# Kernel tuning notes

Measured on AMD Instinct MI355X. Metric: run time of the kernel, lower is better.

The kernel has to match this reference:

```python
import jax, jax.numpy as jnp
import numpy as np

B, S, DIM = 4, 3968, 512
H, HD = 8, 64
CHUNK, NPM, MEM = 496, 32, 1024  # MEM == NPM + 2*CHUNK (required by module's EMA update broadcast)


def _lin(k, din, dout):
    kw, kb = jax.random.split(k)
    w = jax.random.normal(kw, (din, dout), jnp.float32) / np.sqrt(din)
    b = jax.random.normal(kb, (dout,), jnp.float32) * 0.01
    return w, b


def setup_inputs() -> dict:
    key = jax.random.key(0)
    ks = jax.random.split(key, 12)
    inp = {}
    inp["x"] = jax.random.normal(ks[0], (B, S, DIM), jnp.float32)
    inp["persistent_memory"] = jax.random.normal(ks[1], (NPM, DIM), jnp.float32)
    # outer query projection
    inp["Wq_out"], inp["bq_out"] = _lin(ks[2], DIM, DIM)
    # NeuralMemory projections
    inp["mk_w"], inp["mk_b"] = _lin(ks[3], DIM, DIM)
    inp["mv_w"], inp["mv_b"] = _lin(ks[4], DIM, DIM)
    inp["mq_w"], inp["mq_b"] = _lin(ks[5], DIM, DIM)
    # TitanAttention (standard MHA: q/k/v to H*HD, out proj back to DIM)
    inp["aq_w"], inp["aq_b"] = _lin(ks[6], DIM, H * HD)
    inp["ak_w"], inp["ak_b"] = _lin(ks[7], DIM, H * HD)
    inp["av_w"], inp["av_b"] = _lin(ks[8], DIM, H * HD)
    inp["ao_w"], inp["ao_b"] = _lin(ks[9], H * HD, DIM)
    return inp


def reference(x, persistent_memory, Wq_out, bq_out,
              mk_w, mk_b, mv_w, mv_b, mq_w, mq_b,
              aq_w, aq_b, ak_w, ak_b, av_w, av_b, ao_w, ao_b):
    Bn, Sn, D = x.shape
    nch = Sn // CHUNK
    inv_sqrt_d = 1.0 / np.sqrt(D).astype(np.float32)
    inv_sqrt_hd = 1.0 / np.sqrt(HD).astype(np.float32)

    def retrieve(mem, q):
        # mem: [B, MEM, D], q: [B, L, D]
        qp = q @ mq_w + mq_b
        k = mem @ mk_w + mk_b
        v = mem @ mv_w + mv_b
        sc = jnp.einsum('bqd,bmd->bqm', qp, k) * inv_sqrt_d
        a = jax.nn.softmax(sc, axis=-1)
        return jnp.einsum('bqm,bmd->bqd', a, v)

    def mha(t):
        # t: [B, L, D] -> [B, L, D]; dropout inactive (eval)
        Bm, L, _ = t.shape
        q = (t @ aq_w + aq_b).reshape(Bm, L, H, HD)
        k = (t @ ak_w + ak_b).reshape(Bm, L, H, HD)
        v = (t @ av_w + av_b).reshape(Bm, L, H, HD)
        sc = jnp.einsum('bqhd,bkhd->bhqk', q, k) * inv_sqrt_hd
        a = jax.nn.softmax(sc, axis=-1)
        o = jnp.einsum('bhqk,bkhd->bqhd', a, v).reshape(Bm, L, H * HD)
        return o @ ao_w + ao_b

    pm = jnp.broadcast_to(persistent_memory[None], (Bn, NPM, D))
    chunks = x.reshape(Bn, nch, CHUNK, D).transpose(1, 0, 2, 3)  # [nch, B, C, D]
    mem0 = jnp.zeros((Bn, MEM, D), x.dtype)

    def step(mem, chunk):
        query = chunk @ Wq_out + bq_out
        hist = retrieve(mem, query)                              # [B, C, D]
        combined = jnp.concatenate([pm, hist, chunk], axis=1)    # [B, MEM, D]
        attended = mha(combined)
        mem2 = 0.9 * mem + 0.1 * attended                        # EMA update
        mout = retrieve(mem2, attended)
        out = (attended * mout)[:, -CHUNK:]                      # keep last chunk slice
        return mem2, out

    _, outs = jax.lax.scan(step, mem0, chunks)                   # outs: [nch, B, C, D]
    return outs.transpose(1, 0, 2, 3).reshape(Bn, Sn, D)
```

## Files before the change

kernel.cpp:

```cpp
#include <hip/hip_runtime.h>
#include <hip/hip_fp16.h>


typedef __attribute__((ext_vector_type(8))) short short8;
typedef __attribute__((ext_vector_type(4))) float f32x4;

static __device__ __forceinline__ unsigned short f32_bf16(float f) {
  unsigned int u = __float_as_uint(f);
  u += 0x7FFFu + ((u >> 16) & 1u);
  return (unsigned short)(u >> 16);
}
static __device__ __forceinline__ float bf_f32(unsigned short h) {
  return __uint_as_float(((unsigned)h) << 16);
}
static __device__ __forceinline__ unsigned pk(float lo, float hi) {
  return (unsigned)f32_bf16(lo) | ((unsigned)f32_bf16(hi) << 16);
}

template<int BM, int BN, int ATY, int BTY, int CTY, bool GUARD, bool BIAS>
__global__ __launch_bounds__(256) void gemm2(
    const void* __restrict__ Ap, long long Asb, long long Ash, int Ars,
    const void* __restrict__ Bp, long long Bsb, long long Bsh, int Brs,
    void* __restrict__ Cp, long long Csb, long long Csh, int Crs,
    void* __restrict__ Cp2, int csplit, void* __restrict__ Cp3,
    const float* __restrict__ bias, float scale, int M, int Kdim, int Hh)
{
  constexpr int LDP = 72;
  constexpr int WN = (BN >= 128) ? 2 : (BM >= 128 ? 1 : 2);
  constexpr int WM = 4 / WN;
  constexpr int MI = BM / (WM * 16);
  constexpr int NI = BN / (WN * 16);
  constexpr int AP = BM / 32;
  constexpr int BP = BN / 32;

  __shared__ unsigned short As[2][BM][LDP];
  __shared__ unsigned short Bs[2][BN][LDP];

  const int tid  = threadIdx.x;
  const int lane = tid & 63;
  const int w    = tid >> 6;
  const int wm   = w / WN, wn = w % WN;
  const int z    = blockIdx.z;
  const int zb   = z / Hh, zh = z - zb * Hh;
  const int m0   = blockIdx.x * BM;
  const int n0   = blockIdx.y * BN;
  const int lrow = lane & 15;
  const int lkB  = (lane >> 4) * 8;
  const int srow = tid >> 3;
  const int scol = (tid & 7) * 8;

  const float*          Af  = (const float*)Ap          + zb * Asb + zh * Ash;
  const unsigned short* Ahp = (const unsigned short*)Ap + zb * Asb + zh * Ash;
  const float*          Bf  = (const float*)Bp          + zb * Bsb + zh * Bsh;
  const unsigned short* Bhp = (const unsigned short*)Bp + zb * Bsb + zh * Bsh;

  float4 afl[AP][2]; uint4 ahl[AP];
  float4 bfl[BP][2]; uint4 bhl[BP];

  auto loadT = [&](int k0) {
    #pragma unroll
    for (int p = 0; p < AP; ++p) {
      const int row = srow + p * 32;
      const bool ok = !GUARD || (m0 + row) < M;
      if constexpr (ATY == 0) {
        if (ok) {
          const float* s = Af + (long long)(m0 + row) * Ars + k0 + scol;
          afl[p][0] = *(const float4*)s;
          afl[p][1] = *(const float4*)(s + 4);
        } else {
          afl[p][0] = make_float4(0.f,0.f,0.f,0.f);
          afl[p][1] = make_float4(0.f,0.f,0.f,0.f);
        }
      } else {
        ahl[p] = ok ? *(const uint4*)(Ahp + (long long)(m0 + row) * Ars + k0 + scol)
                    : make_uint4(0u,0u,0u,0u);
      }
    }
    #pragma unroll
    for (int p = 0; p < BP; ++p) {
      const int row = srow + p * 32;
      if constexpr (BTY == 0) {
        const float* s = Bf + (long long)(n0 + row) * Brs + k0 + scol;
        bfl[p][0] = *(const float4*)s;
        bfl[p][1] = *(const float4*)(s + 4);
      } else {
        bhl[p] = *(const uint4*)(Bhp + (long long)(n0 + row) * Brs + k0 + scol);
      }
    }
  };
  auto writeT = [&](int buf) {
    #pragma unroll
    for (int p = 0; p < AP; ++p) {
      const int row = srow + p * 32;
      uint4 u;
      if constexpr (ATY == 0) {
        u.x = pk(afl[p][0].x, afl[p][0].y); u.y = pk(afl[p][0].z, afl[p][0].w);
        u.z = pk(afl[p][1].x, afl[p][1].y); u.w = pk(afl[p][1].z, afl[p][1].w);
      } else u = ahl[p];
      *(uint4*)(&As[buf][row][scol]) = u;
    }
    #pragma unroll
    for (int p = 0; p < BP; ++p) {
      const int row = srow + p * 32;
      uint4 u;
      if constexpr (BTY == 0) {
        u.x = pk(bfl[p][0].x, bfl[p][0].y); u.y = pk(bfl[p][0].z, bfl[p][0].w);
        u.z = pk(bfl[p][1].x, bfl[p][1].y); u.w = pk(bfl[p][1].z, bfl[p][1].w);
      } else u = bhl[p];
      *(uint4*)(&Bs[buf][row][scol]) = u;
    }
  };

  f32x4 acc[MI][NI] = {};

  loadT(0);
  writeT(0);
  __syncthreads();

  const int NT = Kdim >> 6;
  int cur = 0;
  for (int t = 0; t < NT; ++t) {
    const bool more = (t + 1) < NT;
    if (more) loadT((t + 1) << 6);

    short8 a8[MI][2], b8[NI][2];
    #pragma unroll
    for (int mi = 0; mi < MI; ++mi) {
      const unsigned short* r = &As[cur][wm * (MI * 16) + mi * 16 + lrow][lkB];
      a8[mi][0] = *(const short8*)r;
      a8[mi][1] = *(const short8*)(r + 32);
    }
    #pragma unroll
    for (int ni = 0; ni < NI; ++ni) {
      const unsigned short* r = &Bs[cur][wn * (NI * 16) + ni * 16 + lrow][lkB];
      b8[ni][0] = *(const short8*)r;
      b8[ni][1] = *(const short8*)(r + 32);
    }
    #pragma unroll
    for (int kk = 0; kk < 2; ++kk)
      #pragma unroll
      for (int mi = 0; mi < MI; ++mi)
        #pragma unroll
        for (int ni = 0; ni < NI; ++ni)
          acc[mi][ni] = __builtin_amdgcn_mfma_f32_16x16x32_bf16(a8[mi][kk], b8[ni][kk], acc[mi][ni], 0, 0, 0);

    if (more) writeT(cur ^ 1);
    __syncthreads();
    cur ^= 1;
  }

  float*          Cf  = (float*)Cp          + zb * Csb + zh * Csh;
  unsigned short* Chn = (unsigned short*)Cp + zb * Csb + zh * Csh;
  unsigned short* Ch2 = (unsigned short*)Cp2;
  unsigned short* Kb3 = (unsigned short*)Cp3;
  const bool trside = (CTY == 4 || CTY == 5) ? (n0 >= csplit) : false;

  #pragma unroll
  for (int ni = 0; ni < NI; ++ni) {
    const int col = n0 + wn * (NI * 16) + ni * 16 + lrow;
    const float bv = BIAS ? bias[col] : 0.0f;
    #pragma unroll
    for (int mi = 0; mi < MI; ++mi) {
      const int rbase = m0 + wm * (MI * 16) + mi * 16 + ((lane >> 4) << 2);
      if constexpr (CTY == 5) {
        ushort4 vt;
        #pragma unroll
        for (int r = 0; r < 4; ++r) {
          const int row = rbase + r;
          const float proj = acc[mi][ni][r] * scale + bv;
          const long long midx = (long long)row * Crs + col;
          const float v = 0.9f * Cf[midx] + 0.1f * proj;
          Cf[midx] = v;
          if (!trside) Kb3[(long long)row * 512 + col] = f32_bf16(v);
          else ((unsigned short*)&vt)[r] = f32_bf16(v);
        }
        if (trside)
          *(ushort4*)(&Ch2[(long long)(rbase >> 10) * 524288
                           + (long long)(col - csplit) * 1024 + (rbase & 1023)]) = vt;
      } else if constexpr (CTY == 6) {
        const float* ATTp = (const float*)Cp2;
        float* Of = (float*)Cp;
        #pragma unroll
        for (int r = 0; r < 4; ++r) {
          const int row = rbase + r;
          if (row < M) {
            const float v = acc[mi][ni][r] * scale;
            const float a = ATTp[((long long)zb * 496 + row) * 512 + col];
            Of[((long long)zb * 3968 + (long long)csplit * 496 + row) * 512 + col] = v * a;
          }
        }
      } else if constexpr (CTY == 8) {
        float* ATTo = (float*)Cp2;
        #pragma unroll
        for (int r = 0; r < 4; ++r) {
          const int row = rbase + r;
          if (row < M) {
            const float v = acc[mi][ni][r] * scale + bv;
            if (col < csplit)
              Kb3[((long long)zb * 496 + row) * 512 + col] = f32_bf16(v);
            else
              ATTo[((long long)zb * 496 + row) * 512 + (col - csplit)] = v;
          }
        }
      } else if (trside) {
        ushort4 v;
        v.x = f32_bf16(acc[mi][ni][0] * scale + bv);
        v.y = f32_bf16(acc[mi][ni][1] * scale + bv);
        v.z = f32_bf16(acc[mi][ni][2] * scale + bv);
        v.w = f32_bf16(acc[mi][ni][3] * scale + bv);
        *(ushort4*)(&Ch2[(long long)(rbase >> 10) * 524288
                         + (long long)(col - csplit) * 1024 + (rbase & 1023)]) = v;
      } else {
        #pragma unroll
        for (int r = 0; r < 4; ++r) {
          const int row = rbase + r;
          if (!GUARD || row < M) {
            const float v = acc[mi][ni][r] * scale + bv;
            if constexpr (CTY == 0)      Cf [(long long)row * Crs + col] = v;
            else                         Chn[(long long)row * Crs + col] = f32_bf16(v);
          }
        }
      }
    }
  }
}

__global__ __launch_bounds__(256) void flash_mha_ks(
    const unsigned short* __restrict__ QK, const unsigned short* __restrict__ Vt,
    unsigned short* __restrict__ Opart, float* __restrict__ ML)
{
  __shared__ unsigned short Ks[128][72];
  __shared__ unsigned short Vs[64][136];
  __shared__ unsigned short Ps[64][136];

  const int tid = threadIdx.x, lane = tid & 63, w = tid >> 6;
  const int f = blockIdx.x;
  const int xcd = f & 7, j = f >> 3;
  const int bh = xcd + 8 * (j >> 5);
  const int jj = j & 31;
  const int qt = jj >> 1, part = jj & 1;
  const int b = bh >> 3, h = bh & 7;
  const int q0 = qt * 64, koff = part * 4;
  const unsigned short* Qp = QK + (long long)b * 1048576 + h * 64;
  const unsigned short* Kp = Qp + 512;
  const unsigned short* Vp = Vt + (long long)b * 524288 + (long long)(h * 64) * 1024;

  const int lr = lane & 15, g = lane >> 4, lk = g * 8;
  const int wq = w * 16;

  short8 qb[2];
  qb[0] = *(const short8*)(Qp + (long long)(q0 + wq + lr) * 1024 + lk);
  qb[1] = *(const short8*)(Qp + (long long)(q0 + wq + lr) * 1024 + 32 + lk);

  const int krow = tid >> 1, kcol = (tid & 1) * 32;
  const int vrow = tid >> 2, vcol = (tid & 3) * 32;

  uint4 kl[4], vl[4];
  auto loadKV = [&](int kt) {
    #pragma unroll
    for (int jx = 0; jx < 4; ++jx)
      kl[jx] = *(const uint4*)(Kp + (long long)(kt * 128 + krow) * 1024 + kcol + jx * 8);
    #pragma unroll
    for (int jx = 0; jx < 4; ++jx)
      vl[jx] = *(const uint4*)(Vp + (long long)vrow * 1024 + kt * 128 + vcol + jx * 8);
  };
  auto writeKV = [&]() {
    #pragma unroll
    for (int jx = 0; jx < 4; ++jx) *(uint4*)(&Ks[krow][kcol + jx * 8]) = kl[jx];
    #pragma unroll
    for (int jx = 0; jx < 4; ++jx) *(uint4*)(&Vs[vrow][vcol + jx * 8]) = vl[jx];
  };

  loadKV(koff); writeKV();
  __syncthreads();

  f32x4 acc[4] = {};
  float m = -1e30f, l = 0.f;

  for (int it = 0; it < 4; ++it) {
    const bool more = it < 3;
    if (more) loadKV(koff + it + 1);

    f32x4 s[8] = {};
    #pragma unroll
    for (int ks = 0; ks < 2; ++ks)
      #pragma unroll
      for (int ni = 0; ni < 8; ++ni) {
        const short8 ka = *(const short8*)(&Ks[ni * 16 + lr][ks * 32 + lk]);
        s[ni] = __builtin_amdgcn_mfma_f32_16x16x32_bf16(ka, qb[ks], s[ni], 0, 0, 0);
      }

    float rm = -1e30f;
    #pragma unroll
    for (int ni = 0; ni < 8; ++ni)
      #pragma unroll
      for (int r = 0; r < 4; ++r) { s[ni][r] *= 0.125f; rm = fmaxf(rm, s[ni][r]); }
    rm = fmaxf(rm, __shfl_xor(rm, 16));
    rm = fmaxf(rm, __shfl_xor(rm, 32));

    const float mn = fmaxf(m, rm);
    const float al = __expf(m - mn);
    m = mn;
    float ls = 0.f;
    #pragma unroll
    for (int ni = 0; ni < 8; ++ni)
      #pragma unroll
      for (int r = 0; r < 4; ++r) { s[ni][r] = __expf(s[ni][r] - m); ls += s[ni][r]; }
    ls += __shfl_xor(ls, 16);
    ls += __shfl_xor(ls, 32);
    l = l * al + ls;
    #pragma unroll
    for (int nd = 0; nd < 4; ++nd)
      #pragma unroll
      for (int r = 0; r < 4; ++r) acc[nd][r] *= al;

    #pragma unroll
    for (int ni = 0; ni < 8; ++ni)
      #pragma unroll
      for (int r = 0; r < 4; ++r)
        Ps[wq + lr][ni * 16 + (g << 2) + r] = f32_bf16(s[ni][r]);

    #pragma unroll
    for (int ks2 = 0; ks2 < 4; ++ks2) {
      const short8 pb = *(const short8*)(&Ps[wq + lr][ks2 * 32 + lk]);
      #pragma unroll
      for (int nd = 0; nd < 4; ++nd) {
        const short8 va = *(const short8*)(&Vs[nd * 16 + lr][ks2 * 32 + lk]);
        acc[nd] = __builtin_amdgcn_mfma_f32_16x16x32_bf16(va, pb, acc[nd], 0, 0, 0);
      }
    }

    if (more) { __syncthreads(); writeKV(); __syncthreads(); }
  }

  const int pbq = (bh * 16 + qt) * 2 + part;
  unsigned short* Ob = Opart + (long long)pbq * 4096;
  #pragma unroll
  for (int nd = 0; nd < 4; ++nd)
    #pragma unroll
    for (int r = 0; r < 4; ++r)
      Ob[(16 * nd + 4 * g + r) * 64 + wq + lr] = f32_bf16(acc[nd][r]);
  if (g == 0) {
    ML[pbq * 128 + wq + lr] = m;
    ML[pbq * 128 + 64 + wq + lr] = l;
  }
}

__global__ __launch_bounds__(256) void combine_mha(
    const unsigned short* __restrict__ Opart, const float* __restrict__ ML,
    unsigned short* __restrict__ OH)
{
  __shared__ float Oc[64][65];
  __shared__ float w1s[64], w2s[64], wis[64];
  const int t = threadIdx.x;
  const int bq = blockIdx.x;
  const int bh = bq >> 4, qt = bq & 15, b = bh >> 3, h = bh & 7, q0 = qt * 64;
  const unsigned short* O1 = Opart + (long long)(bq * 2 + 0) * 4096;
  const unsigned short* O2 = Opart + (long long)(bq * 2 + 1) * 4096;
  const float* ml1 = ML + (bq * 2 + 0) * 128;
  const float* ml2 = ML + (bq * 2 + 1) * 128;
  if (t < 64) {
    const float m1 = ml1[t], l1 = ml1[64 + t], m2 = ml2[t], l2 = ml2[64 + t];
    const float mm = fmaxf(m1, m2);
    const float e1 = __expf(m1 - mm), e2 = __expf(m2 - mm);
    w1s[t] = e1; w2s[t] = e2; wis[t] = 1.0f / (e1 * l1 + e2 * l2);
  }
  __syncthreads();
  {
    const int d = t >> 2, qs = (t & 3) * 16;
    const uint4 a0 = *(const uint4*)(O1 + d * 64 + qs);
    const uint4 a1 = *(const uint4*)(O1 + d * 64 + qs + 8);
    const uint4 b0 = *(const uint4*)(O2 + d * 64 + qs);
    const uint4 b1 = *(const uint4*)(O2 + d * 64 + qs + 8);
    const unsigned short* pa = (const unsigned short*)&a0;
    unsigned short ua[16], ub[16];
    *(uint4*)&ua[0] = a0; *(uint4*)&ua[8] = a1;
    *(uint4*)&ub[0] = b0; *(uint4*)&ub[8] = b1;
    #pragma unroll
    for (int i = 0; i < 16; ++i) {
      const int q = qs + i;
      Oc[d][q] = (w1s[q] * bf_f32(ua[i]) + w2s[q] * bf_f32(ub[i])) * wis[q];
    }
  }
  __syncthreads();
  {
    const int q = t >> 2, ds = (t & 3) * 16;
    unsigned short tmp[16];
    #pragma unroll
    for (int i = 0; i < 16; ++i) tmp[i] = f32_bf16(Oc[ds + i][q]);
    unsigned short* dst = OH + (long long)b * 524288 + (long long)(q0 + q) * 512 + h * 64 + ds;
    *(uint4*)dst = *(uint4*)&tmp[0];
    *(uint4*)(dst + 8) = *(uint4*)&tmp[8];
  }
}

struct TP7 { const float* s[7]; unsigned short* d[7]; };
__global__ __launch_bounds__(256) void transpose7(TP7 tp)
{
  __shared__ float tile[32][33];
  const float* in = tp.s[blockIdx.z];
  unsigned short* out = tp.d[blockIdx.z];
  const int c0 = blockIdx.x * 32, r0 = blockIdx.y * 32;
  const int xx = threadIdx.x & 31, ys = threadIdx.x >> 5;
  #pragma unroll
  for (int yy = ys; yy < 32; yy += 8)
    tile[yy][xx] = in[(long long)(r0 + yy) * 512 + c0 + xx];
  __syncthreads();
  #pragma unroll
  for (int yy = ys; yy < 32; yy += 8)
    out[(long long)(c0 + yy) * 512 + r0 + xx] = f32_bf16(tile[xx][yy]);
}

__global__ __launch_bounds__(256) void softmax_rows_bf(
    const float* __restrict__ buf, unsigned short* __restrict__ obuf,
    int rowsPerZ, long long zStride)
{
  const int gr   = blockIdx.x * 4 + (threadIdx.x >> 6);
  const int lane = threadIdx.x & 63;
  const int z = gr / rowsPerZ;
  const int i = gr - z * rowsPerZ;
  const float* pf = buf + (long long)z * zStride + (long long)i * 1024 + lane * 16;
  float v[16];
  #pragma unroll
  for (int j = 0; j < 4; ++j) {
    const float4 f = ((const float4*)pf)[j];
    v[4*j+0] = f.x; v[4*j+1] = f.y; v[4*j+2] = f.z; v[4*j+3] = f.w;
  }
  float mx = v[0];
  #pragma unroll
  for (int j = 1; j < 16; ++j) mx = fmaxf(mx, v[j]);
  #pragma unroll
  for (int d = 32; d; d >>= 1) mx = fmaxf(mx, __shfl_xor(mx, d));
  float s = 0.0f;
  #pragma unroll
  for (int j = 0; j < 16; ++j) { v[j] = __expf(v[j] - mx); s += v[j]; }
  #pragma unroll
  for (int d = 32; d; d >>= 1) s += __shfl_xor(s, d);
  const float inv = 1.0f / s;
  unsigned short* ph = obuf + (long long)z * zStride + (long long)i * 1024 + lane * 16;
  unsigned uu[8];
  #pragma unroll
  for (int j = 0; j < 8; ++j) uu[j] = pk(v[2*j] * inv, v[2*j+1] * inv);
  ((uint4*)ph)[0] = make_uint4(uu[0], uu[1], uu[2], uu[3]);
  ((uint4*)ph)[1] = make_uint4(uu[4], uu[5], uu[6], uu[7]);
}

__global__ __launch_bounds__(256) void copy_pm8(const float* __restrict__ pm, unsigned short* __restrict__ comb8)
{
  const int ci = blockIdx.y;
  const int idx = blockIdx.x * 256 + threadIdx.x;
  const int b = idx >> 11, e = idx & 2047;
  const int row = e >> 6, d8 = (e & 63) * 8;
  const float* s = pm + row * 512 + d8;
  const float4 f0 = *(const float4*)s;
  const float4 f1 = *(const float4*)(s + 4);
  uint4 u; u.x = pk(f0.x, f0.y); u.y = pk(f0.z, f0.w); u.z = pk(f1.x, f1.y); u.w = pk(f1.z, f1.w);
  *(uint4*)(comb8 + (long long)ci * 2097152 + (long long)b * 524288 + row * 512 + d8) = u;
}

__global__ __launch_bounds__(256) void copy_chunk8(const float* __restrict__ x, unsigned short* __restrict__ comb8)
{
  const int ci = blockIdx.y;
  const int idx = blockIdx.x * 256 + threadIdx.x;
  const int b = idx / 31744, e = idx % 31744;
  const int row = e >> 6, d8 = (e & 63) * 8;
  const float* s = x + ((long long)b * 3968 + ci * 496 + row) * 512 + d8;
  const float4 f0 = *(const float4*)s;
  const float4 f1 = *(const float4*)(s + 4);
  uint4 u; u.x = pk(f0.x, f0.y); u.y = pk(f0.z, f0.w); u.z = pk(f1.x, f1.y); u.w = pk(f1.z, f1.w);
  *(uint4*)(comb8 + (long long)ci * 2097152 + (long long)b * 524288 + (528 + row) * 512 + d8) = u;
}

__global__ __launch_bounds__(256) void init_kv(const float* __restrict__ mkb, const float* __restrict__ mvb,
                                               float* __restrict__ master, unsigned short* __restrict__ Kb)
{
  const int idx = blockIdx.x * 256 + threadIdx.x;
  const int c4 = (idx & 255) * 4;
  const long long row = idx >> 8;
  const float4 v = *(const float4*)((c4 < 512) ? (mkb + c4) : (mvb + c4 - 512));
  *(float4*)(master + row * 1024 + c4) = v;
  if (c4 < 512) {
    ushort4 h; h.x = f32_bf16(v.x); h.y = f32_bf16(v.y); h.z = f32_bf16(v.z); h.w = f32_bf16(v.w);
    *(ushort4*)(Kb + row * 512 + c4) = h;
  }
}

__global__ __launch_bounds__(256) void init_vt(const float* __restrict__ mvb, unsigned short* __restrict__ VT)
{
  const int idx = blockIdx.x * 256 + threadIdx.x;
  const int k8 = (idx & 127) * 8;
  const int d  = (idx >> 7) & 511;
  const int b  = idx >> 16;
  const unsigned short hv = f32_bf16(mvb[d]);
  const ushort4 h4 = make_ushort4(hv, hv, hv, hv);
  unsigned short* dst = VT + (long long)b * 524288 + (long long)d * 1024 + k8;
  *(ushort4*)dst = h4; *(ushort4*)(dst + 4) = h4;
}

__global__ __launch_bounds__(256) void fuse_bias(const float* __restrict__ bq, const float* __restrict__ mq,
                                                 const float* __restrict__ mqb, float* __restrict__ bqm)
{
  const int c = blockIdx.x * 256 + threadIdx.x;
  float s = mqb[c];
  for (int j = 0; j < 512; ++j) s += bq[j] * mq[j * 512 + c];
  bqm[c] = s;
}

__global__ __launch_bounds__(256) void fuse_bias2(const float* __restrict__ aob,
                                                  const float* __restrict__ mkw, const float* __restrict__ mkb,
                                                  const float* __restrict__ mvw, const float* __restrict__ mvb,
                                                  float* __restrict__ baokv)
{
  const int c = blockIdx.x * 256 + threadIdx.x;
  const float* w  = (c < 512) ? mkw : mvw;
  const float* bb = (c < 512) ? mkb : mvb;
  const int cc = c & 511;
  float s = bb[cc];
  for (int j = 0; j < 512; ++j) s += aob[j] * w[j * 512 + cc];
  baokv[c] = s;
}

extern "C" void kernel_launch(void* const* d_in, const int* in_sizes, int n_in,
                              void* d_out, int out_size, void* d_ws, size_t ws_size,
                              hipStream_t stream)
{
  (void)in_sizes; (void)n_in; (void)out_size; (void)ws_size;
  const float* x   = (const float*)d_in[0];
  const float* pm  = (const float*)d_in[1];
  const float* Wq  = (const float*)d_in[2];
  const float* bq  = (const float*)d_in[3];
  const float* mkw = (const float*)d_in[4];
  const float* mkb = (const float*)d_in[5];
  const float* mvw = (const float*)d_in[6];
  const float* mvb = (const float*)d_in[7];
  const float* mqw = (const float*)d_in[8];
  const float* mqb = (const float*)d_in[9];
  const float* aqw = (const float*)d_in[10];
  const float* aqb = (const float*)d_in[11];
  const float* akw = (const float*)d_in[12];
  const float* akb = (const float*)d_in[13];
  const float* avw = (const float*)d_in[14];
  const float* avb = (const float*)d_in[15];
  const float* aow = (const float*)d_in[16];
  const float* aob = (const float*)d_in[17];
  float* out = (float*)d_out;

  char* wsp = (char*)d_ws;
  size_t off = 0;
  auto alloc = [&](size_t b) -> void* { void* p = wsp + off; off += (b + 255) & ~(size_t)255; return p; };

  unsigned short* WTmq  = (unsigned short*)alloc(524288);
  unsigned short* WKV   = (unsigned short*)alloc(1048576);
  unsigned short* WQKV  = (unsigned short*)alloc(1572864);
  unsigned short* Wqm   = (unsigned short*)alloc(524288);
  unsigned short* WaoKV = (unsigned short*)alloc(1048576);
  unsigned short* WQA   = (unsigned short*)alloc(1048576);
  float* bqkv  = (float*)alloc(6144);
  float* bqm   = (float*)alloc(2048);
  float* baokv = (float*)alloc(4096);
  float* bqa   = (float*)alloc(4096);
  float*          master = (float*)alloc(16777216);
  unsigned short* Kb   = (unsigned short*)alloc(4194304);
  unsigned short* VT   = (unsigned short*)alloc(4194304);
  unsigned short* VTm  = (unsigned short*)alloc(4194304);
  unsigned short* QP1  = (unsigned short*)alloc(16252928);
  unsigned short* QP   = (unsigned short*)alloc(2031616);
  unsigned short* comb8= (unsigned short*)alloc(33554432);
  unsigned short* QKb  = (unsigned short*)alloc(8388608);
  unsigned short* OH   = (unsigned short*)alloc(4194304);
  float*          ATT  = (float*)alloc(4063232);
  float*          SC   = (float*)alloc(8126464);
  unsigned short* SCb  = (unsigned short*)alloc(4063232);
  unsigned short* Opart= (unsigned short*)alloc(8388608);
  float*          ML   = (float*)alloc(524288);

  const long long XBS = 2031616, BS = 524288, QBS = 253952;
  const long long SCB = 507904;
  const float sr = 0.044194173824159216f;

  TP7 tp;
  tp.s[0] = mqw; tp.d[0] = WTmq;
  tp.s[1] = mkw; tp.d[1] = WKV;
  tp.s[2] = mvw; tp.d[2] = WKV + 262144;
  tp.s[3] = aqw; tp.d[3] = WQKV;
  tp.s[4] = akw; tp.d[4] = WQKV + 262144;
  tp.s[5] = avw; tp.d[5] = WQKV + 524288;
  tp.s[6] = aow; tp.d[6] = WQA + 262144;
  transpose7<<<dim3(16,16,7),256,0,stream>>>(tp);
  gemm2<64,64,1,0,2,false,false><<<dim3(8,8,1),256,0,stream>>>(
    WTmq, 0, 0, 512, Wq, 0, 0, 512, Wqm, 0, 0, 512,
    nullptr, 0, nullptr, nullptr, 1.0f, 512, 512, 1);
  gemm2<64,64,1,0,2,false,false><<<dim3(16,8,1),256,0,stream>>>(
    WKV, 0, 0, 512, aow, 0, 0, 512, WaoKV, 0, 0, 512,
    nullptr, 0, nullptr, nullptr, 1.0f, 1024, 512, 1);
  gemm2<64,64,1,0,2,false,false><<<dim3(8,8,1),256,0,stream>>>(
    WTmq, 0, 0, 512, aow, 0, 0, 512, WQA, 0, 0, 512,
    nullptr, 0, nullptr, nullptr, 1.0f, 512, 512, 1);
  fuse_bias<<<2,256,0,stream>>>(bq, mqw, mqb, bqm);
  fuse_bias<<<2,256,0,stream>>>(aob, mqw, mqb, bqa);
  fuse_bias2<<<4,256,0,stream>>>(aob, mkw, mkb, mvw, mvb, baokv);
  hipMemcpyAsync(bqa + 512, aob, 2048, hipMemcpyDeviceToDevice, stream);
  gemm2<128,64,0,1,2,false,true><<<dim3(124,8,1),256,0,stream>>>(
    x, 0, 0, 512, Wqm, 0, 0, 512,
    QP1, 0, 0, 512, nullptr, 0, nullptr, bqm, 1.0f, 15872, 512, 1);
  hipMemcpyAsync(bqkv,       aqb, 2048, hipMemcpyDeviceToDevice, stream);
  hipMemcpyAsync(bqkv + 512, akb, 2048, hipMemcpyDeviceToDevice, stream);
  hipMemcpyAsync(bqkv +1024, avb, 2048, hipMemcpyDeviceToDevice, stream);
  init_kv<<<4096,256,0,stream>>>(mkb, mvb, master, Kb);
  init_vt<<<1024,256,0,stream>>>(mvb, VT);
  copy_pm8<<<dim3(32,8),256,0,stream>>>(pm, comb8);
  copy_chunk8<<<dim3(496,8),256,0,stream>>>(x, comb8);

  for (int ci = 0; ci < 8; ++ci) {
    unsigned short* comb = comb8 + (long long)ci * 2097152;

    gemm2<64,64,1,1,0,true,false><<<dim3(8,16,4),256,0,stream>>>(
      QP1 + (long long)ci * 253952, XBS, 0, 512, Kb, BS, 0, 512,
      SC, SCB, 0, 1024, nullptr, 0, nullptr, nullptr, sr, 496, 512, 1);
    softmax_rows_bf<<<496,256,0,stream>>>(SC, SCb, 496, SCB);
    gemm2<64,64,1,1,2,true,false><<<dim3(8,8,4),256,0,stream>>>(
      SCb, SCB, 0, 1024, VT, BS, 0, 1024,
      comb + 32 * 512, BS, 0, 512, nullptr, 0, nullptr, nullptr, 1.0f, 496, 1024, 1);

    gemm2<128,64,1,1,4,false,true><<<dim3(32,24,1),256,0,stream>>>(
      comb, 0, 0, 512, WQKV, 0, 0, 512,
      QKb, 0, 0, 1024, VTm, 1024, nullptr, bqkv, 1.0f, 4096, 512, 1);
    flash_mha_ks<<<1024,256,0,stream>>>(QKb, VTm, Opart, ML);
    combine_mha<<<512,256,0,stream>>>(Opart, ML, OH);

    gemm2<128,64,1,1,5,false,true><<<dim3(32,16,1),256,0,stream>>>(
      OH, 0, 0, 512, WaoKV, 0, 0, 512,
      master, 0, 0, 1024, VT, 512, Kb, baokv, 1.0f, 4096, 512, 1);
    gemm2<64,64,1,1,8,true,true><<<dim3(8,16,4),256,0,stream>>>(
      OH + 528 * 512, BS, 0, 512, WQA, 0, 0, 512,
      nullptr, 0, 0, 512, ATT, 512, QP, bqa, 1.0f, 496, 512, 1);

    gemm2<64,64,1,1,0,true,false><<<dim3(8,16,4),256,0,stream>>>(
      QP, QBS, 0, 512, Kb, BS, 0, 512,
      SC, SCB, 0, 1024, nullptr, 0, nullptr, nullptr, sr, 496, 512, 1);
    softmax_rows_bf<<<496,256,0,stream>>>(SC, SCb, 496, SCB);
    gemm2<64,64,1,1,6,true,false><<<dim3(8,8,4),256,0,stream>>>(
      SCb, SCB, 0, 1024, VT, BS, 0, 1024,
      out, 0, 0, 512, ATT, ci, nullptr, nullptr, 1.0f, 496, 1024, 1);
  }
}
```

Before: 1.314 ms.

## Batch next chunk's history retrieval with current chunk's output retrieval

Both retrievals read the same updated memory (mem2), so the next chunk's history retrieval is merged with the current chunk's output retrieval. The score GEMM, softmax and PV GEMM now run on 992 stacked query rows drawn from two sources, and a new epilogue routes the second half into the next chunk's combined buffer. This removes three kernel launches per iteration and gives the small GEMMs more blocks. The cost is larger score buffers and extra row-split branching in the loaders and epilogue.

```diff
diff --git a/kernel.cpp b/kernel.cpp
--- a/kernel.cpp
+++ b/kernel.cpp
@@ -17,12 +17,13 @@
   return (unsigned)f32_bf16(lo) | ((unsigned)f32_bf16(hi) << 16);
 }
 
-template<int BM, int BN, int ATY, int BTY, int CTY, bool GUARD, bool BIAS>
+template<int BM, int BN, int ATY, int BTY, int CTY, bool GUARD, bool BIAS, bool ASPL>
 __global__ __launch_bounds__(256) void gemm2(
     const void* __restrict__ Ap, long long Asb, long long Ash, int Ars,
     const void* __restrict__ Bp, long long Bsb, long long Bsh, int Brs,
     void* __restrict__ Cp, long long Csb, long long Csh, int Crs,
     void* __restrict__ Cp2, int csplit, void* __restrict__ Cp3,
+    const void* __restrict__ Ap2, long long Asb2,
     const float* __restrict__ bias, float scale, int M, int Kdim, int Hh)
 {
   constexpr int LDP = 72;
@@ -51,6 +52,7 @@
 
   const float*          Af  = (const float*)Ap          + zb * Asb + zh * Ash;
   const unsigned short* Ahp = (const unsigned short*)Ap + zb * Asb + zh * Ash;
+  const unsigned short* A2h = (const unsigned short*)Ap2 + zb * Asb2;
   const float*          Bf  = (const float*)Bp          + zb * Bsb + zh * Bsh;
   const unsigned short* Bhp = (const unsigned short*)Bp + zb * Bsb + zh * Bsh;
 
@@ -61,10 +63,11 @@
     #pragma unroll
     for (int p = 0; p < AP; ++p) {
       const int row = srow + p * 32;
-      const bool ok = !GUARD || (m0 + row) < M;
+      const int grow = m0 + row;
+      const bool ok = !GUARD || grow < M;
       if constexpr (ATY == 0) {
         if (ok) {
-          const float* s = Af + (long long)(m0 + row) * Ars + k0 + scol;
+          const float* s = Af + (long long)grow * Ars + k0 + scol;
           afl[p][0] = *(const float4*)s;
           afl[p][1] = *(const float4*)(s + 4);
         } else {
@@ -72,8 +75,12 @@
           afl[p][1] = make_float4(0.f,0.f,0.f,0.f);
         }
       } else {
-        ahl[p] = ok ? *(const uint4*)(Ahp + (long long)(m0 + row) * Ars + k0 + scol)
-                    : make_uint4(0u,0u,0u,0u);
+        if (ok) {
+          const unsigned short* src;
+          if (!ASPL || grow < 496) src = Ahp + (long long)grow * Ars;
+          else                     src = A2h + (long long)(grow - 496) * 512;
+          ahl[p] = *(const uint4*)(src + k0 + scol);
+        } else ahl[p] = make_uint4(0u,0u,0u,0u);
       }
     }
     #pragma unroll
@@ -202,6 +209,21 @@
               ATTo[((long long)zb * 496 + row) * 512 + (col - csplit)] = v;
           }
         }
+      } else if constexpr (CTY == 9) {
+        const float* ATTp = (const float*)Cp2;
+        float* Of = (float*)Cp;
+        #pragma unroll
+        for (int r = 0; r < 4; ++r) {
+          const int row = rbase + r;
+          if (row < 496) {
+            const float v = acc[mi][ni][r] * scale;
+            const float a = ATTp[((long long)zb * 496 + row) * 512 + col];
+            Of[((long long)zb * 3968 + (long long)csplit * 496 + row) * 512 + col] = v * a;
+          } else if (row < M) {
+            Kb3[(long long)zb * 524288 + (long long)(32 + row - 496) * 512 + col]
+              = f32_bf16(acc[mi][ni][r] * scale);
+          }
+        }
       } else if (trside) {
         ushort4 v;
         v.x = f32_bf16(acc[mi][ni][0] * scale + bv);
@@ -368,14 +390,11 @@
   __syncthreads();
   {
     const int d = t >> 2, qs = (t & 3) * 16;
-    const uint4 a0 = *(const uint4*)(O1 + d * 64 + qs);
-    const uint4 a1 = *(const uint4*)(O1 + d * 64 + qs + 8);
-    const uint4 b0 = *(const uint4*)(O2 + d * 64 + qs);
-    const uint4 b1 = *(const uint4*)(O2 + d * 64 + qs + 8);
-    const unsigned short* pa = (const unsigned short*)&a0;
     unsigned short ua[16], ub[16];
-    *(uint4*)&ua[0] = a0; *(uint4*)&ua[8] = a1;
-    *(uint4*)&ub[0] = b0; *(uint4*)&ub[8] = b1;
+    *(uint4*)&ua[0] = *(const uint4*)(O1 + d * 64 + qs);
+    *(uint4*)&ua[8] = *(const uint4*)(O1 + d * 64 + qs + 8);
+    *(uint4*)&ub[0] = *(const uint4*)(O2 + d * 64 + qs);
+    *(uint4*)&ub[8] = *(const uint4*)(O2 + d * 64 + qs + 8);
     #pragma unroll
     for (int i = 0; i < 16; ++i) {
       const int q = qs + i;
@@ -569,13 +588,13 @@
   unsigned short* QKb  = (unsigned short*)alloc(8388608);
   unsigned short* OH   = (unsigned short*)alloc(4194304);
   float*          ATT  = (float*)alloc(4063232);
-  float*          SC   = (float*)alloc(8126464);
-  unsigned short* SCb  = (unsigned short*)alloc(4063232);
+  float*          SC   = (float*)alloc(16515072);
+  unsigned short* SCb  = (unsigned short*)alloc(8257536);
   unsigned short* Opart= (unsigned short*)alloc(8388608);
   float*          ML   = (float*)alloc(524288);
 
   const long long XBS = 2031616, BS = 524288, QBS = 253952;
-  const long long SCB = 507904;
+  const long long SCB2 = 1015808;
   const float sr = 0.044194173824159216f;
 
   TP7 tp;
@@ -587,22 +606,22 @@
   tp.s[5] = avw; tp.d[5] = WQKV + 524288;
   tp.s[6] = aow; tp.d[6] = WQA + 262144;
   transpose7<<<dim3(16,16,7),256,0,stream>>>(tp);
-  gemm2<64,64,1,0,2,false,false><<<dim3(8,8,1),256,0,stream>>>(
+  gemm2<64,64,1,0,2,false,false,false><<<dim3(8,8,1),256,0,stream>>>(
     WTmq, 0, 0, 512, Wq, 0, 0, 512, Wqm, 0, 0, 512,
-    nullptr, 0, nullptr, nullptr, 1.0f, 512, 512, 1);
-  gemm2<64,64,1,0,2,false,false><<<dim3(16,8,1),256,0,stream>>>(
+    nullptr, 0, nullptr, nullptr, 0, nullptr, 1.0f, 512, 512, 1);
+  gemm2<64,64,1,0,2,false,false,false><<<dim3(16,8,1),256,0,stream>>>(
     WKV, 0, 0, 512, aow, 0, 0, 512, WaoKV, 0, 0, 512,
-    nullptr, 0, nullptr, nullptr, 1.0f, 1024, 512, 1);
-  gemm2<64,64,1,0,2,false,false><<<dim3(8,8,1),256,0,stream>>>(
+    nullptr, 0, nullptr, nullptr, 0, nullptr, 1.0f, 1024, 512, 1);
+  gemm2<64,64,1,0,2,false,false,false><<<dim3(8,8,1),256,0,stream>>>(
     WTmq, 0, 0, 512, aow, 0, 0, 512, WQA, 0, 0, 512,
-    nullptr, 0, nullptr, nullptr, 1.0f, 512, 512, 1);
+    nullptr, 0, nullptr, nullptr, 0, nullptr, 1.0f, 512, 512, 1);
   fuse_bias<<<2,256,0,stream>>>(bq, mqw, mqb, bqm);
   fuse_bias<<<2,256,0,stream>>>(aob, mqw, mqb, bqa);
   fuse_bias2<<<4,256,0,stream>>>(aob, mkw, mkb, mvw, mvb, baokv);
   hipMemcpyAsync(bqa + 512, aob, 2048, hipMemcpyDeviceToDevice, stream);
-  gemm2<128,64,0,1,2,false,true><<<dim3(124,8,1),256,0,stream>>>(
+  gemm2<128,64,0,1,2,false,true,false><<<dim3(124,8,1),256,0,stream>>>(
     x, 0, 0, 512, Wqm, 0, 0, 512,
-    QP1, 0, 0, 512, nullptr, 0, nullptr, bqm, 1.0f, 15872, 512, 1);
+    QP1, 0, 0, 512, nullptr, 0, nullptr, nullptr, 0, bqm, 1.0f, 15872, 512, 1);
   hipMemcpyAsync(bqkv,       aqb, 2048, hipMemcpyDeviceToDevice, stream);
   hipMemcpyAsync(bqkv + 512, akb, 2048, hipMemcpyDeviceToDevice, stream);
   hipMemcpyAsync(bqkv +1024, avb, 2048, hipMemcpyDeviceToDevice, stream);
@@ -611,36 +630,40 @@
   copy_pm8<<<dim3(32,8),256,0,stream>>>(pm, comb8);
   copy_chunk8<<<dim3(496,8),256,0,stream>>>(x, comb8);
 
+  gemm2<64,64,1,1,0,true,false,false><<<dim3(8,16,4),256,0,stream>>>(
+    QP1, XBS, 0, 512, Kb, BS, 0, 512,
+    SC, SCB2, 0, 1024, nullptr, 0, nullptr, nullptr, 0, nullptr, sr, 496, 512, 1);
+  softmax_rows_bf<<<496,256,0,stream>>>(SC, SCb, 496, SCB2);
+  gemm2<64,64,1,1,2,true,false,false><<<dim3(8,8,4),256,0,stream>>>(
+    SCb, SCB2, 0, 1024, VT, BS, 0, 1024,
+    comb8 + 32 * 512, BS, 0, 512, nullptr, 0, nullptr, nullptr, 0, nullptr, 1.0f, 496, 1024, 1);
+
   for (int ci = 0; ci < 8; ++ci) {
     unsigned short* comb = comb8 + (long long)ci * 2097152;
-
-    gemm2<64,64,1,1,0,true,false><<<dim3(8,16,4),256,0,stream>>>(
-      QP1 + (long long)ci * 253952, XBS, 0, 512, Kb, BS, 0, 512,
-      SC, SCB, 0, 1024, nullptr, 0, nullptr, nullptr, sr, 496, 512, 1);
-    softmax_rows_bf<<<496,256,0,stream>>>(SC, SCb, 496, SCB);
-    gemm2<64,64,1,1,2,true,false><<<dim3(8,8,4),256,0,stream>>>(
-      SCb, SCB, 0, 1024, VT, BS, 0, 1024,
-      comb + 32 * 512, BS, 0, 512, nullptr, 0, nullptr, nullptr, 1.0f, 496, 1024, 1);
-
-    gemm2<128,64,1,1,4,false,true><<<dim3(32,24,1),256,0,stream>>>(
+    const bool last = (ci == 7);
+    const int Mm = last ? 496 : 992;
+
+    gemm2<128,64,1,1,4,false,true,false><<<dim3(32,24,1),256,0,stream>>>(
       comb, 0, 0, 512, WQKV, 0, 0, 512,
-      QKb, 0, 0, 1024, VTm, 1024, nullptr, bqkv, 1.0f, 4096, 512, 1);
+      QKb, 0, 0, 1024, VTm, 1024, nullptr, nullptr, 0, bqkv, 1.0f, 4096, 512, 1);
     flash_mha_ks<<<1024,256,0,stream>>>(QKb, VTm, Opart, ML);
     combine_mha<<<512,256,0,stream>>>(Opart, ML, OH);
 
-    gemm2<128,64,1,1,5,false,true><<<dim3(32,16,1),256,0,stream>>>(
+    gemm2<128,64,1,1,5,false,true,false><<<dim3(32,16,1),256,0,stream>>>(
       OH, 0, 0, 512, WaoKV, 0, 0, 512,
-      master, 0, 0, 1024, VT, 512, Kb, baokv, 1.0f, 4096, 512, 1);
-    gemm2<64,64,1,1,8,true,true><<<dim3(8,16,4),256,0,stream>>>(
+      master, 0, 0, 1024, VT, 512, Kb, nullptr, 0, baokv, 1.0f, 4096, 512, 1);
+    gemm2<64,64,1,1,8,true,true,false><<<dim3(8,16,4),256,0,stream>>>(
       OH + 528 * 512, BS, 0, 512, WQA, 0, 0, 512,
-      nullptr, 0, 0, 512, ATT, 512, QP, bqa, 1.0f, 496, 512, 1);
-
-    gemm2<64,64,1,1,0,true,false><<<dim3(8,16,4),256,0,stream>>>(
+      nullptr, 0, 0, 512, ATT, 512, QP, nullptr, 0, bqa, 1.0f, 496, 512, 1);
+
+    gemm2<64,64,1,1,0,true,false,true><<<dim3(last?8:16,16,4),256,0,stream>>>(
       QP, QBS, 0, 512, Kb, BS, 0, 512,
-      SC, SCB, 0, 1024, nullptr, 0, nullptr, nullptr, sr, 496, 512, 1);
-    softmax_rows_bf<<<496,256,0,stream>>>(SC, SCb, 496, SCB);
-    gemm2<64,64,1,1,6,true,false><<<dim3(8,8,4),256,0,stream>>>(
-      SCb, SCB, 0, 1024, VT, BS, 0, 1024,
-      out, 0, 0, 512, ATT, ci, nullptr, nullptr, 1.0f, 496, 1024, 1);
-  }
-}
+      SC, SCB2, 0, 1024, nullptr, 0, nullptr,
+      QP1 + (long long)(ci + 1) * 253952, XBS, nullptr, sr, Mm, 512, 1);
+    softmax_rows_bf<<<(last?496:992),256,0,stream>>>(SC, SCb, Mm, SCB2);
+    gemm2<64,64,1,1,9,true,false,false><<<dim3(last?8:16,8,4),256,0,stream>>>(
+      SCb, SCB2, 0, 1024, VT, BS, 0, 1024,
+      out, 0, 0, 512, ATT, ci, last ? nullptr : (comb8 + (long long)(ci + 1) * 2097152),
+      nullptr, 0, nullptr, 1.0f, Mm, 1024, 1);
+  }
+}
```

Result: faster. 1.251 ms (-4.8%).
